# Kernel optimization log

Hardware: AMD Instinct MI355X
Metric: run time of the kernel (lower is better)

## Reference

```python
import jax, jax.numpy as jnp
import numpy as np

B, S, D = 2, 2048, 2048
H = 16
KV_RANK = 512
NOPE, ROPE = 128, 64
QK_HD = NOPE + ROPE  # 192
V_HD = 128
SCALE = QK_HD ** -0.5
EPS = 1.1920929e-07  # torch RMSNorm default eps = finfo(fp32).eps
NEG = -1e9


def rmsnorm(x, w):
    return x * jax.lax.rsqrt(jnp.mean(x * x, axis=-1, keepdims=True) + EPS) * w


def apply_rope(x, freqs):
    # x: (b, s, h, r) interleaved pairs; freqs: (s, r//2) angles
    sh = x.shape
    xr = x.reshape(*sh[:-1], -1, 2)
    a, b = xr[..., 0], xr[..., 1]
    cos = jnp.cos(freqs)[None, :, None, :]
    sin = jnp.sin(freqs)[None, :, None, :]
    return jnp.stack([a * cos - b * sin, a * sin + b * cos], axis=-1).reshape(sh)


def setup_inputs() -> dict:
    key = jax.random.key(0)
    ks = jax.random.split(key, 8)
    inv = lambda k, shape, fan_in: jax.random.uniform(k, shape, jnp.float32, -1.0, 1.0) / np.sqrt(fan_in)
    x = jax.random.normal(ks[0], (B, S, D), jnp.float32)
    freqs = jax.random.uniform(ks[1], (S, ROPE // 2), jnp.float32) * np.float32(np.pi)
    mask = jnp.where(jnp.triu(jnp.ones((S, S), bool), k=1), jnp.float32(NEG), jnp.float32(0.0))
    wq_w = inv(ks[2], (H * QK_HD, D), D)
    wq_b = jnp.zeros((H * QK_HD,), jnp.float32)
    wkv_a_w = inv(ks[3], (KV_RANK + ROPE, D), D)
    wkv_a_b = jnp.zeros((KV_RANK + ROPE,), jnp.float32)
    kv_norm_w = jnp.ones((KV_RANK,), jnp.float32)
    wkv_b_w = inv(ks[4], (H * (NOPE + V_HD), KV_RANK), KV_RANK)
    wo_w = inv(ks[5], (D, H * V_HD), H * V_HD)
    wo_b = jnp.zeros((D,), jnp.float32)
    return dict(x=x, freqs=freqs, mask=mask, wq_w=wq_w, wq_b=wq_b,
                wkv_a_w=wkv_a_w, wkv_a_b=wkv_a_b, kv_norm_w=kv_norm_w,
                wkv_b_w=wkv_b_w, wo_w=wo_w, wo_b=wo_b)


def reference(x, freqs, mask, wq_w, wq_b, wkv_a_w, wkv_a_b, kv_norm_w, wkv_b_w, wo_w, wo_b):
    b, s, _ = x.shape
    # q projection (q_lora_rank == 0 path)
    q = (x @ wq_w.T + wq_b).reshape(b, s, H, QK_HD)
    q_nope, q_pe = q[..., :NOPE], q[..., NOPE:]
    q_pe = apply_rope(q_pe, freqs)
    # latent kv projection
    kv = x @ wkv_a_w.T + wkv_a_b
    kv, k_pe = kv[..., :KV_RANK], kv[..., KV_RANK:]
    k_pe = apply_rope(k_pe[:, :, None, :], freqs)[:, :, 0, :]  # (b, t, r)
    kv_proj = rmsnorm(kv, kv_norm_w)  # (b, t, c)
    wkv_b = wkv_b_w.reshape(H, NOPE + V_HD, KV_RANK)
    # absorb K-nope projection into q
    q_nope = jnp.einsum('bshd,hdc->bshc', q_nope, wkv_b[:, :NOPE])
    scores = (jnp.einsum('bshc,btc->bsht', q_nope, kv_proj)
              + jnp.einsum('bshr,btr->bsht', q_pe, k_pe)) * SCALE
    scores = scores + mask[None, :, None, :]
    scores = jax.nn.softmax(scores.astype(jnp.float32), axis=-1).astype(x.dtype)
    out = jnp.einsum('bsht,btc->bshc', scores, kv_proj)
    out = jnp.einsum('bshc,hdc->bshd', out, wkv_b[:, -V_HD:])
    return out.reshape(b, s, H * V_HD) @ wo_w.T + wo_b
```

## Files before the change

### kernel.cpp

```cpp
#include <hip/hip_runtime.h>
#include <hip/hip_bf16.h>
#include <math.h>

#define B_ 2
#define S_ 2048
#define H_ 16
#define SCALE_ 0.07216878364870323f
#define EPS_ 1.1920929e-07f
#define M0_ 8.0f

typedef __attribute__((ext_vector_type(8))) short bf16x8;
typedef __attribute__((ext_vector_type(4))) float f32x4;
union U4 { uint4 u; bf16x8 v; f32x4 f; };

__device__ __forceinline__ uint bfbits(float x) {
    uint u = __float_as_uint(x);
    return (u + 0x7fffu + ((u >> 16) & 1u)) >> 16;
}
__device__ __forceinline__ uint pack2bf(float a, float b) {
    return bfbits(a) | (bfbits(b) << 16);
}
__device__ __forceinline__ void gld_lds16(const ushort* g, ushort* l) {
    __builtin_amdgcn_global_load_lds(
        (const __attribute__((address_space(1))) uint*)g,
        (__attribute__((address_space(3))) uint*)l, 16, 0, 0);
}

template<bool OUT_BF16>
__global__ __launch_bounds__(256) void mgemm(
    const ushort* __restrict__ A, int lda, long long aOff,
    const ushort* __restrict__ Bm, int ldb, long long bOff,
    const float* __restrict__ bias, float scale,
    void* __restrict__ Cv, int ldc, long long cOff, int K)
{
    __shared__ ushort As[128 * 32];
    __shared__ ushort Bs[128 * 32];

    const int z = blockIdx.z;
    A  += (long long)z * aOff;
    Bm += (long long)z * bOff;

    const int n0 = blockIdx.x * 128;
    const int m0 = blockIdx.y * 128;
    const int tid = threadIdx.x;
    const int w   = tid >> 6;
    const int l   = tid & 63;
    const int m   = l & 15;
    const int q4  = l >> 4;
    const int mw  = (w & 1) * 64;
    const int nw  = (w >> 1) * 64;
    const int sr  = l >> 2;
    const int sc  = l & 3;

    f32x4 acc[4][4];
#pragma unroll
    for (int i = 0; i < 4; ++i)
#pragma unroll
        for (int j = 0; j < 4; ++j) acc[i][j] = (f32x4){0.f, 0.f, 0.f, 0.f};

    for (int k0 = 0; k0 < K; k0 += 32) {
#pragma unroll
        for (int jj = 0; jj < 2; ++jj) {
            const int slot = w * 2 + jj;
            const int row  = slot * 16 + sr;
            const int g    = sc ^ ((row >> 1) & 3);
            gld_lds16(&A[(long long)(m0 + row) * lda + k0 + g * 8], &As[slot * 512]);
            gld_lds16(&Bm[(long long)(n0 + row) * ldb + k0 + g * 8], &Bs[slot * 512]);
        }
        __syncthreads();

        U4 af[4], bf[4];
#pragma unroll
        for (int i = 0; i < 4; ++i) {
            const int ra = mw + i * 16 + m;
            af[i].u = *(const uint4*)&As[ra * 32 + (q4 ^ ((ra >> 1) & 3)) * 8];
            const int rb = nw + i * 16 + m;
            bf[i].u = *(const uint4*)&Bs[rb * 32 + (q4 ^ ((rb >> 1) & 3)) * 8];
        }
#pragma unroll
        for (int i = 0; i < 4; ++i)
#pragma unroll
            for (int j = 0; j < 4; ++j)
                acc[i][j] = __builtin_amdgcn_mfma_f32_16x16x32_bf16(
                    af[i].v, bf[j].v, acc[i][j], 0, 0, 0);
        __syncthreads();
    }

#pragma unroll
    for (int j = 0; j < 4; ++j) {
        const int cn = n0 + nw + j * 16 + m;
        const float bv = bias ? bias[cn] : 0.0f;
#pragma unroll
        for (int i = 0; i < 4; ++i) {
            const int rw = m0 + mw + i * 16 + q4 * 4;
#pragma unroll
            for (int r = 0; r < 4; ++r) {
                const float val = acc[i][j][r] * scale + bv;
                if (OUT_BF16)
                    ((ushort*)Cv)[(long long)z * cOff + (long long)(rw + r) * ldc + cn] =
                        (ushort)bfbits(val);
                else
                    ((float*)Cv)[(long long)z * cOff + (long long)(rw + r) * ldc + cn] = val;
            }
        }
    }
}

__global__ __launch_bounds__(256) void conv_bf16(
    const float* __restrict__ s, ushort* __restrict__ d)
{
    const long long i = ((long long)blockIdx.x * 256 + threadIdx.x) * 4;
    float4 v = *(const float4*)&s[i];
    uint2 p; p.x = pack2bf(v.x, v.y); p.y = pack2bf(v.z, v.w);
    *(uint2*)&d[i] = p;
}

__global__ __launch_bounds__(256) void conv_wkva(
    const float* __restrict__ s, ushort* __restrict__ d)
{
    const int i = (blockIdx.x * 256 + threadIdx.x) * 4;
    const int r = i >> 11;
    uint2 p = make_uint2(0u, 0u);
    if (r < 576) {
        float4 v = *(const float4*)&s[i];
        p.x = pack2bf(v.x, v.y); p.y = pack2bf(v.z, v.w);
    }
    *(uint2*)&d[i] = p;
}

__global__ __launch_bounds__(256) void conv_wkvb_half(
    const float* __restrict__ Wsrc, ushort* __restrict__ V, int rowoff)
{
    const int i = (blockIdx.x * 256 + threadIdx.x) * 4;
    const int h = i >> 16;
    const int rem = i & 65535;
    float4 v = *(const float4*)&Wsrc[((long long)(h * 256 + rowoff)) * 512 + rem];
    uint2 p; p.x = pack2bf(v.x, v.y); p.y = pack2bf(v.z, v.w);
    *(uint2*)&V[i] = p;
}

__global__ __launch_bounds__(256) void conv_qn192(
    const float* __restrict__ q_raw, ushort* __restrict__ q192)
{
    const int i = (blockIdx.x * 256 + threadIdx.x) * 4;
    const int bs = i >> 11;
    const int c = i & 2047;
    const int hh = c >> 7, d = c & 127;
    float4 v = *(const float4*)&q_raw[(long long)bs * 3072 + hh * 192 + d];
    uint2 p;
    p.x = pack2bf(v.x * SCALE_, v.y * SCALE_);
    p.y = pack2bf(v.z * SCALE_, v.w * SCALE_);
    *(uint2*)&q192[((long long)bs * 16 + hh) * 192 + d] = p;
}

__global__ __launch_bounds__(256) void rope_q_kernel(
    const float* __restrict__ q_raw, const float* __restrict__ freqs,
    ushort* __restrict__ q192)
{
    const int idx = blockIdx.x * 256 + threadIdx.x;
    const int i = idx & 31;
    const int h = (idx >> 5) & 15;
    const int s = (idx >> 9) & 2047;
    const int b = idx >> 20;
    const float f = freqs[s * 32 + i];
    float cs, sn;
    __sincosf(f, &sn, &cs);
    const int row = (b * S_ + s) * H_ + h;
    const float a  = q_raw[(long long)(b * S_ + s) * 3072 + h * 192 + 128 + 2 * i];
    const float bb = q_raw[(long long)(b * S_ + s) * 3072 + h * 192 + 128 + 2 * i + 1];
    *(uint*)&q192[(long long)row * 192 + 128 + 2 * i] =
        pack2bf((a * cs - bb * sn) * SCALE_, (a * sn + bb * cs) * SCALE_);
}

__global__ __launch_bounds__(64) void kv_post_kernel(
    const float* __restrict__ kv_raw, const float* __restrict__ bias,
    const float* __restrict__ w, const float* __restrict__ freqs,
    ushort* __restrict__ kv_h)
{
    const int bs = blockIdx.x;
    const int lane = threadIdx.x;
    const float* src = kv_raw + (long long)bs * 640;
    ushort* dst = kv_h + (long long)bs * 576;

    const int c = 4 * lane;
    float4 v0 = *(const float4*)&src[c];
    float4 v1 = *(const float4*)&src[256 + c];
    float4 b0 = *(const float4*)&bias[c];
    float4 b1 = *(const float4*)&bias[256 + c];
    v0.x += b0.x; v0.y += b0.y; v0.z += b0.z; v0.w += b0.w;
    v1.x += b1.x; v1.y += b1.y; v1.z += b1.z; v1.w += b1.w;
    float ss = v0.x * v0.x + v0.y * v0.y + v0.z * v0.z + v0.w * v0.w +
               v1.x * v1.x + v1.y * v1.y + v1.z * v1.z + v1.w * v1.w;
#pragma unroll
    for (int o = 32; o; o >>= 1) ss += __shfl_xor(ss, o, 64);
    const float rs = rsqrtf(ss * (1.0f / 512.0f) + EPS_);

    float4 w0 = *(const float4*)&w[c];
    float4 w1 = *(const float4*)&w[256 + c];
    uint2 p0, p1;
    p0.x = pack2bf(v0.x * rs * w0.x, v0.y * rs * w0.y);
    p0.y = pack2bf(v0.z * rs * w0.z, v0.w * rs * w0.w);
    p1.x = pack2bf(v1.x * rs * w1.x, v1.y * rs * w1.y);
    p1.y = pack2bf(v1.z * rs * w1.z, v1.w * rs * w1.w);
    *(uint2*)&dst[c] = p0;
    *(uint2*)&dst[256 + c] = p1;

    if (lane < 32) {
        const int s = bs & 2047;
        const float f = freqs[s * 32 + lane];
        float cs, sn;
        __sincosf(f, &sn, &cs);
        const float a  = src[512 + 2 * lane]     + bias[512 + 2 * lane];
        const float b2 = src[512 + 2 * lane + 1] + bias[512 + 2 * lane + 1];
        *(uint*)&dst[512 + 2 * lane] = pack2bf(a * cs - b2 * sn, a * sn + b2 * cs);
    }
}

__global__ __launch_bounds__(256) void prep_kimg(
    const ushort* __restrict__ K_h, uint4* __restrict__ khimg)
{
    const int g = blockIdx.x * 256 + threadIdx.x;
    const int lane = g & 63, ck = (g >> 6) & 7, h = (g >> 9) & 15;
    const int tile = (g >> 13) & 63, b = g >> 19;
    const int m = lane & 15, q4 = lane >> 4, f = ck >> 1, s = ck & 1;
    const uint4 v = *(const uint4*)&K_h[
        ((long long)(b * S_ + tile * 32 + s * 16 + m)) * 2048 + h * 128 + f * 32 + q4 * 8];
    khimg[(((long long)(b * 64 + tile) * 16 + h) * 8 + ck) * 64 + lane] = v;
}

__global__ __launch_bounds__(256) void prep_vimg(
    const ushort* __restrict__ V_hT, uint4* __restrict__ vhimg)
{
    const int g = blockIdx.x * 256 + threadIdx.x;
    const int lane = g & 63, c = (g >> 6) & 7, h = (g >> 9) & 15;
    const int tile = (g >> 13) & 63, b = g >> 19;
    const int m = lane & 15, q4 = lane >> 4;
    const uint4 v = *(const uint4*)&V_hT[
        ((long long)((b * 16 + h) * 128 + c * 16 + m)) * 2048 + tile * 32 + q4 * 8];
    vhimg[(((long long)(b * 64 + tile) * 16 + h) * 8 + c) * 64 + lane] = v;
}

__global__ __launch_bounds__(256) void prep_rimg(
    const ushort* __restrict__ kv_h, uint4* __restrict__ rimg)
{
    const int g = blockIdx.x * 256 + threadIdx.x;
    const int lane = g & 63, ck = (g >> 6) & 3, tile = (g >> 8) & 63, b = g >> 14;
    const int m = lane & 15, q4 = lane >> 4, f2 = ck >> 1, s = ck & 1;
    const uint4 v = *(const uint4*)&kv_h[
        ((long long)(b * S_ + tile * 32 + s * 16 + m)) * 576 + 512 + f2 * 32 + q4 * 8];
    rimg[((long long)(b * 64 + tile) * 4 + ck) * 64 + lane] = v;
}

__global__ __launch_bounds__(256, 2) void attn_kernel(
    const ushort* __restrict__ q192,
    const uint4*  __restrict__ khimg,
    const uint4*  __restrict__ rimg,
    const uint4*  __restrict__ vhimg,
    ushort* __restrict__ o_h)
{
    __shared__ uint buf[2][20 * 256];

    const int p    = blockIdx.x;
    const int h    = blockIdx.y;
    const int b    = blockIdx.z;
    const int tid  = threadIdx.x;
    const int wid  = tid >> 6;
    const int lane = tid & 63;
    const int m    = lane & 15;
    const int q4   = lane >> 4;

    auto stage = [&](int bs, int it) {
        const long long tb = (long long)(b * 64 + it);
        const uint4* kb = khimg + ((tb * 16 + h) * 8) * 64;
        const uint4* rb = rimg  + (tb * 4) * 64;
        const uint4* vb = vhimg + ((tb * 16 + h) * 8) * 64;
        ushort* l = (ushort*)&buf[bs][0];
        gld_lds16((const ushort*)(kb + (wid    ) * 64 + lane), l + (wid     ) * 512);
        gld_lds16((const ushort*)(kb + (wid + 4) * 64 + lane), l + (wid +  4) * 512);
        gld_lds16((const ushort*)(rb + (wid    ) * 64 + lane), l + (wid +  8) * 512);
        gld_lds16((const ushort*)(vb + (wid    ) * 64 + lane), l + (wid + 12) * 512);
        gld_lds16((const ushort*)(vb + (wid + 4) * 64 + lane), l + (wid + 16) * 512);
    };

    int cur = 0;
    for (int pass = 0; pass < 2; ++pass) {
        const int chunk = pass ? p : (31 - p);
        const int row0  = chunk * 64 + wid * 16;
        const int sRow  = row0 + m;

        U4 qf[6];
        {
            const uint4* qp = (const uint4*)(q192 + ((long long)(b * S_ + sRow) * H_ + h) * 192);
#pragma unroll
            for (int f = 0; f < 6; ++f) qf[f].u = qp[f * 4 + q4];
        }

        f32x4 o[8];
#pragma unroll
        for (int c = 0; c < 8; ++c) o[c] = (f32x4){0.f, 0.f, 0.f, 0.f};
        float lacc = 0.0f;

        const int nT = chunk * 2 + 2;
        __syncthreads();
        stage(cur, 0);

        for (int it = 0; it < nT; ++it) {
            const int t0 = it * 32;
            __syncthreads();
            if (it + 1 < nT) stage(cur ^ 1, it + 1);
            __builtin_amdgcn_sched_barrier(0);

            if (t0 <= row0 + 15) {
                const uint* bb0 = &buf[cur][0];
                const int abase = lane * 4;

                f32x4 st0 = (f32x4){0.f, 0.f, 0.f, 0.f};
                f32x4 st1 = (f32x4){0.f, 0.f, 0.f, 0.f};
                const bool skip1 = (t0 >= row0);
                if (!skip1) {
#pragma unroll
                    for (int f = 0; f < 6; ++f) {
                        const int ck = (f < 4) ? f * 2 : (f - 4) * 2 + 8;
                        U4 a0, a1;
                        a0.u = *(const uint4*)&bb0[ck * 256 + abase];
                        a1.u = *(const uint4*)&bb0[(ck + 1) * 256 + abase];
                        st0 = __builtin_amdgcn_mfma_f32_16x16x32_bf16(a0.v, qf[f].v, st0, 0, 0, 0);
                        st1 = __builtin_amdgcn_mfma_f32_16x16x32_bf16(a1.v, qf[f].v, st1, 0, 0, 0);
                    }
                } else {
#pragma unroll
                    for (int f = 0; f < 6; ++f) {
                        const int ck = (f < 4) ? f * 2 : (f - 4) * 2 + 8;
                        U4 a0;
                        a0.u = *(const uint4*)&bb0[ck * 256 + abase];
                        st0 = __builtin_amdgcn_mfma_f32_16x16x32_bf16(a0.v, qf[f].v, st0, 0, 0, 0);
                    }
                }

                const int tb0 = t0 + q4 * 4;
                const int tb1 = t0 + 16 + q4 * 4;
                float p00 = (tb0 + 0 <= sRow) ? __expf(st0[0] - M0_) : 0.0f;
                float p01 = (tb0 + 1 <= sRow) ? __expf(st0[1] - M0_) : 0.0f;
                float p02 = (tb0 + 2 <= sRow) ? __expf(st0[2] - M0_) : 0.0f;
                float p03 = (tb0 + 3 <= sRow) ? __expf(st0[3] - M0_) : 0.0f;
                float p10 = (tb1 + 0 <= sRow) ? __expf(st1[0] - M0_) : 0.0f;
                float p11 = (tb1 + 1 <= sRow) ? __expf(st1[1] - M0_) : 0.0f;
                float p12 = (tb1 + 2 <= sRow) ? __expf(st1[2] - M0_) : 0.0f;
                float p13 = (tb1 + 3 <= sRow) ? __expf(st1[3] - M0_) : 0.0f;
                lacc += (p00 + p01) + (p02 + p03) + (p10 + p11) + (p12 + p13);

                U4 bb;
                {
                    uint pk00 = pack2bf(p00, p01);
                    uint pk01 = pack2bf(p02, p03);
                    uint pk10 = pack2bf(p10, p11);
                    uint pk11 = pack2bf(p12, p13);
                    const int srcA = ((lane >> 4) & 1) * 32 + m;
                    const int srcB = srcA + 16;
                    uint a00 = (uint)__shfl((int)pk00, srcA, 64);
                    uint a01 = (uint)__shfl((int)pk01, srcA, 64);
                    uint a10 = (uint)__shfl((int)pk10, srcA, 64);
                    uint a11 = (uint)__shfl((int)pk11, srcA, 64);
                    uint b00 = (uint)__shfl((int)pk00, srcB, 64);
                    uint b01 = (uint)__shfl((int)pk01, srcB, 64);
                    uint b10 = (uint)__shfl((int)pk10, srcB, 64);
                    uint b11 = (uint)__shfl((int)pk11, srcB, 64);
                    const bool hi2 = (lane >> 5) & 1;
                    bb.u.x = hi2 ? a10 : a00;
                    bb.u.y = hi2 ? a11 : a01;
                    bb.u.z = hi2 ? b10 : b00;
                    bb.u.w = hi2 ? b11 : b01;
                }

#pragma unroll
                for (int c = 0; c < 8; ++c) {
                    U4 av; av.u = *(const uint4*)&bb0[(12 + c) * 256 + abase];
                    o[c] = __builtin_amdgcn_mfma_f32_16x16x32_bf16(av.v, bb.v, o[c], 0, 0, 0);
                }
            }
            cur ^= 1;
        }

        lacc += __shfl_xor(lacc, 16, 64);
        lacc += __shfl_xor(lacc, 32, 64);
        const float inv = 1.0f / lacc;

        ushort* op = o_h + ((long long)(b * S_ + sRow) * H_ + h) * 128;
#pragma unroll
        for (int c = 0; c < 8; ++c) {
            uint2 pv;
            pv.x = pack2bf(o[c][0] * inv, o[c][1] * inv);
            pv.y = pack2bf(o[c][2] * inv, o[c][3] * inv);
            *(uint2*)&op[c * 16 + q4 * 4] = pv;
        }
    }
}

extern "C" void kernel_launch(void* const* d_in, const int* in_sizes, int n_in,
                              void* d_out, int out_size, void* d_ws, size_t ws_size,
                              hipStream_t stream)
{
    const float* x         = (const float*)d_in[0];
    const float* freqs     = (const float*)d_in[1];
    const float* wq_w      = (const float*)d_in[3];
    const float* wq_b      = (const float*)d_in[4];
    const float* wkv_a_w   = (const float*)d_in[5];
    const float* wkv_a_b   = (const float*)d_in[6];
    const float* kv_norm_w = (const float*)d_in[7];
    const float* wkv_b_w   = (const float*)d_in[8];
    const float* wo_w      = (const float*)d_in[9];
    const float* wo_b      = (const float*)d_in[10];
    float* out = (float*)d_out;

    char* w = (char*)d_ws;
    ushort* x_bf    = (ushort*)w;  w += 16777216;
    ushort* wq_bf   = (ushort*)w;  w += 12582912;
    ushort* wkva_bf = (ushort*)w;  w += 2621440;
    ushort* wo_bf   = (ushort*)w;  w += 8388608;
    ushort* wkvbK   = (ushort*)w;  w += 2097152;
    ushort* wkvbV   = (ushort*)w;  w += 2097152;
    float*  kv_raw  = (float*)w;   w += 10485760;
    ushort* kv_h    = (ushort*)w;  w += 4718592;
    ushort* K_h     = (ushort*)w;  w += 16777216;
    ushort* V_hT    = (ushort*)w;  w += 16777216;
    uint4*  khimg   = (uint4*)w;   w += 16777216;
    uint4*  vhimg   = (uint4*)w;   w += 16777216;
    uint4*  rimg    = (uint4*)w;   w += 524288;
    char* RA = w;                  w += 50331648;
    float*  q_raw = (float*)RA;
    ushort* o_h   = (ushort*)RA;
    ushort* q192  = (ushort*)w;    w += 25165824;

    dim3 blk(256);

    conv_bf16 <<<dim3(8192), blk, 0, stream>>>(x, x_bf);
    conv_bf16 <<<dim3(6144), blk, 0, stream>>>(wq_w, wq_bf);
    conv_wkva <<<dim3(1280), blk, 0, stream>>>(wkv_a_w, wkva_bf);
    conv_bf16 <<<dim3(4096), blk, 0, stream>>>(wo_w, wo_bf);
    conv_wkvb_half<<<dim3(1024), blk, 0, stream>>>(wkv_b_w, wkvbK, 0);
    conv_wkvb_half<<<dim3(1024), blk, 0, stream>>>(wkv_b_w, wkvbV, 128);

    mgemm<false><<<dim3(24, 32, 1), blk, 0, stream>>>(
        x_bf, 2048, 0LL, wq_bf, 2048, 0LL, wq_b, 1.0f, q_raw, 3072, 0LL, 2048);

    mgemm<false><<<dim3(5, 32, 1), blk, 0, stream>>>(
        x_bf, 2048, 0LL, wkva_bf, 2048, 0LL, nullptr, 1.0f, kv_raw, 640, 0LL, 2048);

    rope_q_kernel<<<dim3(8192), blk, 0, stream>>>(q_raw, freqs, q192);
    conv_qn192<<<dim3(8192), blk, 0, stream>>>(q_raw, q192);

    kv_post_kernel<<<dim3(4096), dim3(64), 0, stream>>>(
        kv_raw, wkv_a_b, kv_norm_w, freqs, kv_h);

    for (int b = 0; b < 2; ++b) {
        mgemm<true><<<dim3(1, 16, 16), blk, 0, stream>>>(
            kv_h + (long long)b * S_ * 576, 576, 0LL,
            wkvbK, 512, 65536LL, nullptr, 1.0f,
            K_h + (long long)b * S_ * 2048, 2048, 128LL, 512);
        mgemm<true><<<dim3(16, 1, 16), blk, 0, stream>>>(
            wkvbV, 512, 65536LL,
            kv_h + (long long)b * S_ * 576, 576, 0LL, nullptr, 1.0f,
            V_hT + (long long)b * 16 * 128 * 2048, 2048, 262144LL, 512);
    }

    prep_kimg<<<dim3(4096), blk, 0, stream>>>(K_h, khimg);
    prep_vimg<<<dim3(4096), blk, 0, stream>>>(V_hT, vhimg);
    prep_rimg<<<dim3(128),  blk, 0, stream>>>(kv_h, rimg);

    attn_kernel<<<dim3(16, 16, 2), blk, 0, stream>>>(q192, khimg, rimg, vhimg, o_h);

    mgemm<false><<<dim3(16, 32, 1), blk, 0, stream>>>(
        o_h, 2048, 0LL, wo_bf, 2048, 0LL, wo_b, 1.0f, out, 2048, 0LL, 2048);
}
```

Baseline: 509.4 us.

## Merge prep kernels, batch GEMMs, and process two row tiles per attention block

Six conversion kernels become one launch, as do the three image-prep kernels and the two q-prep kernels. The per-batch K/V GEMM loop becomes one launch each by giving the GEMM a two-level z offset. The attention kernel now has each wave process two 16-row groups (64 rows apart) over a 128-row chunk, so each staged K/V tile is reused by twice as many rows. It also folds log2(e) into the q scale to use exp2f, uses the hardware bf16 pack instruction, and schedules the largest chunks first. The cost is higher register pressure in attention and a different causal load-balancing scheme.

```diff
diff --git a/kernel.cpp b/kernel.cpp
--- a/kernel.cpp
+++ b/kernel.cpp
@@ -6,6 +6,7 @@
 #define S_ 2048
 #define H_ 16
 #define SCALE_ 0.07216878364870323f
+#define SL2_ (0.07216878364870323f * 1.4426950408889634f)
 #define EPS_ 1.1920929e-07f
 #define M0_ 8.0f
 
@@ -19,6 +20,11 @@
 }
 __device__ __forceinline__ uint pack2bf(float a, float b) {
     return bfbits(a) | (bfbits(b) << 16);
+}
+__device__ __forceinline__ uint cvtpk(float a, float b) {
+    uint r;
+    asm("v_cvt_pk_bf16_f32 %0, %1, %2" : "=v"(r) : "v"(a), "v"(b));
+    return r;
 }
 __device__ __forceinline__ void gld_lds16(const ushort* g, ushort* l) {
     __builtin_amdgcn_global_load_lds(
@@ -28,17 +34,20 @@
 
 template<bool OUT_BF16>
 __global__ __launch_bounds__(256) void mgemm(
-    const ushort* __restrict__ A, int lda, long long aOff,
-    const ushort* __restrict__ Bm, int ldb, long long bOff,
+    const ushort* __restrict__ A, int lda, long long aOff1, long long aOff2,
+    const ushort* __restrict__ Bm, int ldb, long long bOff1, long long bOff2,
     const float* __restrict__ bias, float scale,
-    void* __restrict__ Cv, int ldc, long long cOff, int K)
+    void* __restrict__ Cv, int ldc, long long cOff1, long long cOff2,
+    int K, int zDiv)
 {
     __shared__ ushort As[128 * 32];
     __shared__ ushort Bs[128 * 32];
 
     const int z = blockIdx.z;
-    A  += (long long)z * aOff;
-    Bm += (long long)z * bOff;
+    const int z1 = z % zDiv, z2 = z / zDiv;
+    A  += z1 * aOff1 + z2 * aOff2;
+    Bm += z1 * bOff1 + z2 * bOff2;
+    const long long cBase = z1 * cOff1 + z2 * cOff2;
 
     const int n0 = blockIdx.x * 128;
     const int m0 = blockIdx.y * 128;
@@ -97,79 +106,94 @@
             for (int r = 0; r < 4; ++r) {
                 const float val = acc[i][j][r] * scale + bv;
                 if (OUT_BF16)
-                    ((ushort*)Cv)[(long long)z * cOff + (long long)(rw + r) * ldc + cn] =
+                    ((ushort*)Cv)[cBase + (long long)(rw + r) * ldc + cn] =
                         (ushort)bfbits(val);
                 else
-                    ((float*)Cv)[(long long)z * cOff + (long long)(rw + r) * ldc + cn] = val;
+                    ((float*)Cv)[cBase + (long long)(rw + r) * ldc + cn] = val;
             }
         }
     }
 }
 
-__global__ __launch_bounds__(256) void conv_bf16(
-    const float* __restrict__ s, ushort* __restrict__ d)
-{
-    const long long i = ((long long)blockIdx.x * 256 + threadIdx.x) * 4;
-    float4 v = *(const float4*)&s[i];
-    uint2 p; p.x = pack2bf(v.x, v.y); p.y = pack2bf(v.z, v.w);
-    *(uint2*)&d[i] = p;
-}
-
-__global__ __launch_bounds__(256) void conv_wkva(
-    const float* __restrict__ s, ushort* __restrict__ d)
-{
-    const int i = (blockIdx.x * 256 + threadIdx.x) * 4;
-    const int r = i >> 11;
-    uint2 p = make_uint2(0u, 0u);
-    if (r < 576) {
-        float4 v = *(const float4*)&s[i];
-        p.x = pack2bf(v.x, v.y); p.y = pack2bf(v.z, v.w);
-    }
-    *(uint2*)&d[i] = p;
-}
-
-__global__ __launch_bounds__(256) void conv_wkvb_half(
-    const float* __restrict__ Wsrc, ushort* __restrict__ V, int rowoff)
-{
-    const int i = (blockIdx.x * 256 + threadIdx.x) * 4;
-    const int h = i >> 16;
-    const int rem = i & 65535;
-    float4 v = *(const float4*)&Wsrc[((long long)(h * 256 + rowoff)) * 512 + rem];
-    uint2 p; p.x = pack2bf(v.x, v.y); p.y = pack2bf(v.z, v.w);
-    *(uint2*)&V[i] = p;
-}
-
-__global__ __launch_bounds__(256) void conv_qn192(
-    const float* __restrict__ q_raw, ushort* __restrict__ q192)
-{
-    const int i = (blockIdx.x * 256 + threadIdx.x) * 4;
-    const int bs = i >> 11;
-    const int c = i & 2047;
-    const int hh = c >> 7, d = c & 127;
-    float4 v = *(const float4*)&q_raw[(long long)bs * 3072 + hh * 192 + d];
-    uint2 p;
-    p.x = pack2bf(v.x * SCALE_, v.y * SCALE_);
-    p.y = pack2bf(v.z * SCALE_, v.w * SCALE_);
-    *(uint2*)&q192[((long long)bs * 16 + hh) * 192 + d] = p;
-}
-
-__global__ __launch_bounds__(256) void rope_q_kernel(
+__global__ __launch_bounds__(256) void conv_all(
+    const float* __restrict__ x, const float* __restrict__ wq,
+    const float* __restrict__ wkva, const float* __restrict__ wo,
+    const float* __restrict__ wkvb,
+    ushort* __restrict__ x_bf, ushort* __restrict__ wq_bf,
+    ushort* __restrict__ wkva_bf, ushort* __restrict__ wo_bf,
+    ushort* __restrict__ wkvbK, ushort* __restrict__ wkvbV)
+{
+    const int bid = blockIdx.x;
+    const int tid = threadIdx.x;
+    if (bid < 8192) {
+        const long long i = ((long long)bid * 256 + tid) * 4;
+        float4 v = *(const float4*)&x[i];
+        uint2 p; p.x = pack2bf(v.x, v.y); p.y = pack2bf(v.z, v.w);
+        *(uint2*)&x_bf[i] = p;
+    } else if (bid < 14336) {
+        const long long i = ((long long)(bid - 8192) * 256 + tid) * 4;
+        float4 v = *(const float4*)&wq[i];
+        uint2 p; p.x = pack2bf(v.x, v.y); p.y = pack2bf(v.z, v.w);
+        *(uint2*)&wq_bf[i] = p;
+    } else if (bid < 15616) {
+        const int i = ((bid - 14336) * 256 + tid) * 4;
+        const int r = i >> 11;
+        uint2 p = make_uint2(0u, 0u);
+        if (r < 576) {
+            float4 v = *(const float4*)&wkva[i];
+            p.x = pack2bf(v.x, v.y); p.y = pack2bf(v.z, v.w);
+        }
+        *(uint2*)&wkva_bf[i] = p;
+    } else if (bid < 19712) {
+        const long long i = ((long long)(bid - 15616) * 256 + tid) * 4;
+        float4 v = *(const float4*)&wo[i];
+        uint2 p; p.x = pack2bf(v.x, v.y); p.y = pack2bf(v.z, v.w);
+        *(uint2*)&wo_bf[i] = p;
+    } else if (bid < 20736) {
+        const int i = ((bid - 19712) * 256 + tid) * 4;
+        const int h = i >> 16, rem = i & 65535;
+        float4 v = *(const float4*)&wkvb[((long long)(h * 256)) * 512 + rem];
+        uint2 p; p.x = pack2bf(v.x, v.y); p.y = pack2bf(v.z, v.w);
+        *(uint2*)&wkvbK[i] = p;
+    } else {
+        const int i = ((bid - 20736) * 256 + tid) * 4;
+        const int h = i >> 16, rem = i & 65535;
+        float4 v = *(const float4*)&wkvb[((long long)(h * 256 + 128)) * 512 + rem];
+        uint2 p; p.x = pack2bf(v.x, v.y); p.y = pack2bf(v.z, v.w);
+        *(uint2*)&wkvbV[i] = p;
+    }
+}
+
+__global__ __launch_bounds__(256) void qprep(
     const float* __restrict__ q_raw, const float* __restrict__ freqs,
     ushort* __restrict__ q192)
 {
     const int idx = blockIdx.x * 256 + threadIdx.x;
-    const int i = idx & 31;
-    const int h = (idx >> 5) & 15;
-    const int s = (idx >> 9) & 2047;
-    const int b = idx >> 20;
-    const float f = freqs[s * 32 + i];
-    float cs, sn;
-    __sincosf(f, &sn, &cs);
-    const int row = (b * S_ + s) * H_ + h;
-    const float a  = q_raw[(long long)(b * S_ + s) * 3072 + h * 192 + 128 + 2 * i];
-    const float bb = q_raw[(long long)(b * S_ + s) * 3072 + h * 192 + 128 + 2 * i + 1];
-    *(uint*)&q192[(long long)row * 192 + 128 + 2 * i] =
-        pack2bf((a * cs - bb * sn) * SCALE_, (a * sn + bb * cs) * SCALE_);
+    const int row = idx / 48;
+    const int c4  = idx % 48;
+    const int bs = row >> 4, h = row & 15;
+    const float* src = q_raw + (long long)bs * 3072 + h * 192;
+    if (c4 < 32) {
+        const int d = c4 * 4;
+        float4 v = *(const float4*)&src[d];
+        uint2 p;
+        p.x = pack2bf(v.x * SL2_, v.y * SL2_);
+        p.y = pack2bf(v.z * SL2_, v.w * SL2_);
+        *(uint2*)&q192[(long long)row * 192 + d] = p;
+    } else {
+        const int j = c4 - 32;
+        const int s = bs & 2047;
+        const float f0 = freqs[s * 32 + j * 2];
+        const float f1 = freqs[s * 32 + j * 2 + 1];
+        float c0, s0, c1, s1;
+        __sincosf(f0, &s0, &c0);
+        __sincosf(f1, &s1, &c1);
+        float4 v = *(const float4*)&src[128 + j * 4];
+        uint2 p;
+        p.x = pack2bf((v.x * c0 - v.y * s0) * SL2_, (v.x * s0 + v.y * c0) * SL2_);
+        p.y = pack2bf((v.z * c1 - v.w * s1) * SL2_, (v.z * s1 + v.w * c1) * SL2_);
+        *(uint2*)&q192[(long long)row * 192 + 128 + j * 4] = p;
+    }
 }
 
 __global__ __launch_bounds__(64) void kv_post_kernel(
@@ -216,39 +240,37 @@
     }
 }
 
-__global__ __launch_bounds__(256) void prep_kimg(
-    const ushort* __restrict__ K_h, uint4* __restrict__ khimg)
-{
-    const int g = blockIdx.x * 256 + threadIdx.x;
-    const int lane = g & 63, ck = (g >> 6) & 7, h = (g >> 9) & 15;
-    const int tile = (g >> 13) & 63, b = g >> 19;
-    const int m = lane & 15, q4 = lane >> 4, f = ck >> 1, s = ck & 1;
-    const uint4 v = *(const uint4*)&K_h[
-        ((long long)(b * S_ + tile * 32 + s * 16 + m)) * 2048 + h * 128 + f * 32 + q4 * 8];
-    khimg[(((long long)(b * 64 + tile) * 16 + h) * 8 + ck) * 64 + lane] = v;
-}
-
-__global__ __launch_bounds__(256) void prep_vimg(
-    const ushort* __restrict__ V_hT, uint4* __restrict__ vhimg)
-{
-    const int g = blockIdx.x * 256 + threadIdx.x;
-    const int lane = g & 63, c = (g >> 6) & 7, h = (g >> 9) & 15;
-    const int tile = (g >> 13) & 63, b = g >> 19;
-    const int m = lane & 15, q4 = lane >> 4;
-    const uint4 v = *(const uint4*)&V_hT[
-        ((long long)((b * 16 + h) * 128 + c * 16 + m)) * 2048 + tile * 32 + q4 * 8];
-    vhimg[(((long long)(b * 64 + tile) * 16 + h) * 8 + c) * 64 + lane] = v;
-}
-
-__global__ __launch_bounds__(256) void prep_rimg(
-    const ushort* __restrict__ kv_h, uint4* __restrict__ rimg)
-{
-    const int g = blockIdx.x * 256 + threadIdx.x;
-    const int lane = g & 63, ck = (g >> 6) & 3, tile = (g >> 8) & 63, b = g >> 14;
-    const int m = lane & 15, q4 = lane >> 4, f2 = ck >> 1, s = ck & 1;
-    const uint4 v = *(const uint4*)&kv_h[
-        ((long long)(b * S_ + tile * 32 + s * 16 + m)) * 576 + 512 + f2 * 32 + q4 * 8];
-    rimg[((long long)(b * 64 + tile) * 4 + ck) * 64 + lane] = v;
+__global__ __launch_bounds__(256) void prep_all(
+    const ushort* __restrict__ K_h, const ushort* __restrict__ V_hT,
+    const ushort* __restrict__ kv_h,
+    uint4* __restrict__ khimg, uint4* __restrict__ vhimg,
+    uint4* __restrict__ rimg)
+{
+    const int bid = blockIdx.x;
+    if (bid < 4096) {
+        const int g = bid * 256 + threadIdx.x;
+        const int lane = g & 63, ck = (g >> 6) & 7, h = (g >> 9) & 15;
+        const int tile = (g >> 13) & 63, b = g >> 19;
+        const int m = lane & 15, q4 = lane >> 4, f = ck >> 1, s = ck & 1;
+        const uint4 v = *(const uint4*)&K_h[
+            ((long long)(b * S_ + tile * 32 + s * 16 + m)) * 2048 + h * 128 + f * 32 + q4 * 8];
+        khimg[(((long long)(b * 64 + tile) * 16 + h) * 8 + ck) * 64 + lane] = v;
+    } else if (bid < 8192) {
+        const int g = (bid - 4096) * 256 + threadIdx.x;
+        const int lane = g & 63, c = (g >> 6) & 7, h = (g >> 9) & 15;
+        const int tile = (g >> 13) & 63, b = g >> 19;
+        const int m = lane & 15, q4 = lane >> 4;
+        const uint4 v = *(const uint4*)&V_hT[
+            ((long long)((b * 16 + h) * 128 + c * 16 + m)) * 2048 + tile * 32 + q4 * 8];
+        vhimg[(((long long)(b * 64 + tile) * 16 + h) * 8 + c) * 64 + lane] = v;
+    } else {
+        const int g = (bid - 8192) * 256 + threadIdx.x;
+        const int lane = g & 63, ck = (g >> 6) & 3, tile = (g >> 8) & 63, b = g >> 14;
+        const int m = lane & 15, q4 = lane >> 4, f2 = ck >> 1, s = ck & 1;
+        const uint4 v = *(const uint4*)&kv_h[
+            ((long long)(b * S_ + tile * 32 + s * 16 + m)) * 576 + 512 + f2 * 32 + q4 * 8];
+        rimg[((long long)(b * 64 + tile) * 4 + ck) * 64 + lane] = v;
+    }
 }
 
 __global__ __launch_bounds__(256, 2) void attn_kernel(
@@ -260,14 +282,20 @@
 {
     __shared__ uint buf[2][20 * 256];
 
-    const int p    = blockIdx.x;
-    const int h    = blockIdx.y;
-    const int b    = blockIdx.z;
+    const int hb   = blockIdx.x;
+    const int h    = hb & 15;
+    const int b    = hb >> 4;
+    const int chunk = 15 - (int)blockIdx.y;
     const int tid  = threadIdx.x;
     const int wid  = tid >> 6;
     const int lane = tid & 63;
     const int m    = lane & 15;
     const int q4   = lane >> 4;
+
+    const int row0a = chunk * 128 + wid * 16;
+    const int row0b = row0a + 64;
+    const int sRa   = row0a + m;
+    const int sRb   = row0b + m;
 
     auto stage = [&](int bs, int it) {
         const long long tb = (long long)(b * 64 + it);
@@ -282,117 +310,157 @@
         gld_lds16((const ushort*)(vb + (wid + 4) * 64 + lane), l + (wid + 16) * 512);
     };
 
+    U4 qfa[6], qfb[6];
+    {
+        const uint4* qpa = (const uint4*)(q192 + ((long long)(b * S_ + sRa) * H_ + h) * 192);
+        const uint4* qpb = (const uint4*)(q192 + ((long long)(b * S_ + sRb) * H_ + h) * 192);
+#pragma unroll
+        for (int f = 0; f < 6; ++f) { qfa[f].u = qpa[f * 4 + q4]; qfb[f].u = qpb[f * 4 + q4]; }
+    }
+
+    f32x4 oA[8], oB[8];
+#pragma unroll
+    for (int c = 0; c < 8; ++c) {
+        oA[c] = (f32x4){0.f, 0.f, 0.f, 0.f};
+        oB[c] = (f32x4){0.f, 0.f, 0.f, 0.f};
+    }
+    float lA = 0.0f, lB = 0.0f;
+
+    auto softpack = [&](const f32x4 s0, const f32x4 s1, int t0v, int rw0,
+                        float& lac) -> U4 {
+        float p00, p01, p02, p03, p10, p11, p12, p13;
+        if (t0v + 31 <= rw0) {
+            p00 = exp2f(s0[0] - M0_); p01 = exp2f(s0[1] - M0_);
+            p02 = exp2f(s0[2] - M0_); p03 = exp2f(s0[3] - M0_);
+            p10 = exp2f(s1[0] - M0_); p11 = exp2f(s1[1] - M0_);
+            p12 = exp2f(s1[2] - M0_); p13 = exp2f(s1[3] - M0_);
+        } else {
+            const int sR = rw0 + m;
+            const int tb0 = t0v + q4 * 4;
+            const int tb1 = tb0 + 16;
+            p00 = (tb0 + 0 <= sR) ? exp2f(s0[0] - M0_) : 0.0f;
+            p01 = (tb0 + 1 <= sR) ? exp2f(s0[1] - M0_) : 0.0f;
+            p02 = (tb0 + 2 <= sR) ? exp2f(s0[2] - M0_) : 0.0f;
+            p03 = (tb0 + 3 <= sR) ? exp2f(s0[3] - M0_) : 0.0f;
+            p10 = (tb1 + 0 <= sR) ? exp2f(s1[0] - M0_) : 0.0f;
+            p11 = (tb1 + 1 <= sR) ? exp2f(s1[1] - M0_) : 0.0f;
+            p12 = (tb1 + 2 <= sR) ? exp2f(s1[2] - M0_) : 0.0f;
+            p13 = (tb1 + 3 <= sR) ? exp2f(s1[3] - M0_) : 0.0f;
+        }
+        lac += (p00 + p01) + (p02 + p03) + (p10 + p11) + (p12 + p13);
+        U4 bb;
+        {
+            uint pk00 = cvtpk(p00, p01);
+            uint pk01 = cvtpk(p02, p03);
+            uint pk10 = cvtpk(p10, p11);
+            uint pk11 = cvtpk(p12, p13);
+            const int srcA = ((lane >> 4) & 1) * 32 + m;
+            const int srcB = srcA + 16;
+            uint a00 = (uint)__shfl((int)pk00, srcA, 64);
+            uint a01 = (uint)__shfl((int)pk01, srcA, 64);
+            uint a10 = (uint)__shfl((int)pk10, srcA, 64);
+            uint a11 = (uint)__shfl((int)pk11, srcA, 64);
+            uint b00 = (uint)__shfl((int)pk00, srcB, 64);
+            uint b01 = (uint)__shfl((int)pk01, srcB, 64);
+            uint b10 = (uint)__shfl((int)pk10, srcB, 64);
+            uint b11 = (uint)__shfl((int)pk11, srcB, 64);
+            const bool hi2 = (lane >> 5) & 1;
+            bb.u.x = hi2 ? a10 : a00;
+            bb.u.y = hi2 ? a11 : a01;
+            bb.u.z = hi2 ? b10 : b00;
+            bb.u.w = hi2 ? b11 : b01;
+        }
+        return bb;
+    };
+
+    const int nT = chunk * 4 + 4;
+    stage(0, 0);
     int cur = 0;
-    for (int pass = 0; pass < 2; ++pass) {
-        const int chunk = pass ? p : (31 - p);
-        const int row0  = chunk * 64 + wid * 16;
-        const int sRow  = row0 + m;
-
-        U4 qf[6];
-        {
-            const uint4* qp = (const uint4*)(q192 + ((long long)(b * S_ + sRow) * H_ + h) * 192);
-#pragma unroll
-            for (int f = 0; f < 6; ++f) qf[f].u = qp[f * 4 + q4];
-        }
-
-        f32x4 o[8];
-#pragma unroll
-        for (int c = 0; c < 8; ++c) o[c] = (f32x4){0.f, 0.f, 0.f, 0.f};
-        float lacc = 0.0f;
-
-        const int nT = chunk * 2 + 2;
+
+    for (int it = 0; it < nT; ++it) {
+        const int t0 = it * 32;
         __syncthreads();
-        stage(cur, 0);
-
-        for (int it = 0; it < nT; ++it) {
-            const int t0 = it * 32;
-            __syncthreads();
-            if (it + 1 < nT) stage(cur ^ 1, it + 1);
-            __builtin_amdgcn_sched_barrier(0);
-
-            if (t0 <= row0 + 15) {
-                const uint* bb0 = &buf[cur][0];
-                const int abase = lane * 4;
-
-                f32x4 st0 = (f32x4){0.f, 0.f, 0.f, 0.f};
-                f32x4 st1 = (f32x4){0.f, 0.f, 0.f, 0.f};
-                const bool skip1 = (t0 >= row0);
-                if (!skip1) {
-#pragma unroll
-                    for (int f = 0; f < 6; ++f) {
-                        const int ck = (f < 4) ? f * 2 : (f - 4) * 2 + 8;
-                        U4 a0, a1;
-                        a0.u = *(const uint4*)&bb0[ck * 256 + abase];
+        if (it + 1 < nT) stage(cur ^ 1, it + 1);
+        __builtin_amdgcn_sched_barrier(0);
+
+        const uint* bb0 = &buf[cur][0];
+        const int abase = lane * 4;
+        const bool liveB = (t0 <= row0b + 15);
+        const bool liveA = (t0 <= row0a + 15);
+        const bool twoA  = (t0 < row0a);
+        const bool twoB  = (t0 < row0b);
+
+        if (liveB) {
+            f32x4 sA0 = (f32x4){0.f,0.f,0.f,0.f}, sA1 = (f32x4){0.f,0.f,0.f,0.f};
+            f32x4 sB0 = (f32x4){0.f,0.f,0.f,0.f}, sB1 = (f32x4){0.f,0.f,0.f,0.f};
+
+            if (twoA) {
+#pragma unroll
+                for (int f = 0; f < 6; ++f) {
+                    const int ck = (f < 4) ? f * 2 : (f - 4) * 2 + 8;
+                    U4 a0, a1;
+                    a0.u = *(const uint4*)&bb0[ck * 256 + abase];
+                    a1.u = *(const uint4*)&bb0[(ck + 1) * 256 + abase];
+                    sA0 = __builtin_amdgcn_mfma_f32_16x16x32_bf16(a0.v, qfa[f].v, sA0, 0, 0, 0);
+                    sB0 = __builtin_amdgcn_mfma_f32_16x16x32_bf16(a0.v, qfb[f].v, sB0, 0, 0, 0);
+                    sA1 = __builtin_amdgcn_mfma_f32_16x16x32_bf16(a1.v, qfa[f].v, sA1, 0, 0, 0);
+                    sB1 = __builtin_amdgcn_mfma_f32_16x16x32_bf16(a1.v, qfb[f].v, sB1, 0, 0, 0);
+                }
+            } else {
+#pragma unroll
+                for (int f = 0; f < 6; ++f) {
+                    const int ck = (f < 4) ? f * 2 : (f - 4) * 2 + 8;
+                    U4 a0;
+                    a0.u = *(const uint4*)&bb0[ck * 256 + abase];
+                    if (liveA)
+                        sA0 = __builtin_amdgcn_mfma_f32_16x16x32_bf16(a0.v, qfa[f].v, sA0, 0, 0, 0);
+                    sB0 = __builtin_amdgcn_mfma_f32_16x16x32_bf16(a0.v, qfb[f].v, sB0, 0, 0, 0);
+                    if (twoB) {
+                        U4 a1;
                         a1.u = *(const uint4*)&bb0[(ck + 1) * 256 + abase];
-                        st0 = __builtin_amdgcn_mfma_f32_16x16x32_bf16(a0.v, qf[f].v, st0, 0, 0, 0);
-                        st1 = __builtin_amdgcn_mfma_f32_16x16x32_bf16(a1.v, qf[f].v, st1, 0, 0, 0);
-                    }
-                } else {
-#pragma unroll
-                    for (int f = 0; f < 6; ++f) {
-                        const int ck = (f < 4) ? f * 2 : (f - 4) * 2 + 8;
-                        U4 a0;
-                        a0.u = *(const uint4*)&bb0[ck * 256 + abase];
-                        st0 = __builtin_amdgcn_mfma_f32_16x16x32_bf16(a0.v, qf[f].v, st0, 0, 0, 0);
+                        sB1 = __builtin_amdgcn_mfma_f32_16x16x32_bf16(a1.v, qfb[f].v, sB1, 0, 0, 0);
                     }
                 }
-
-                const int tb0 = t0 + q4 * 4;
-                const int tb1 = t0 + 16 + q4 * 4;
-                float p00 = (tb0 + 0 <= sRow) ? __expf(st0[0] - M0_) : 0.0f;
-                float p01 = (tb0 + 1 <= sRow) ? __expf(st0[1] - M0_) : 0.0f;
-                float p02 = (tb0 + 2 <= sRow) ? __expf(st0[2] - M0_) : 0.0f;
-                float p03 = (tb0 + 3 <= sRow) ? __expf(st0[3] - M0_) : 0.0f;
-                float p10 = (tb1 + 0 <= sRow) ? __expf(st1[0] - M0_) : 0.0f;
-                float p11 = (tb1 + 1 <= sRow) ? __expf(st1[1] - M0_) : 0.0f;
-                float p12 = (tb1 + 2 <= sRow) ? __expf(st1[2] - M0_) : 0.0f;
-                float p13 = (tb1 + 3 <= sRow) ? __expf(st1[3] - M0_) : 0.0f;
-                lacc += (p00 + p01) + (p02 + p03) + (p10 + p11) + (p12 + p13);
-
-                U4 bb;
-                {
-                    uint pk00 = pack2bf(p00, p01);
-                    uint pk01 = pack2bf(p02, p03);
-                    uint pk10 = pack2bf(p10, p11);
-                    uint pk11 = pack2bf(p12, p13);
-                    const int srcA = ((lane >> 4) & 1) * 32 + m;
-                    const int srcB = srcA + 16;
-                    uint a00 = (uint)__shfl((int)pk00, srcA, 64);
-                    uint a01 = (uint)__shfl((int)pk01, srcA, 64);
-                    uint a10 = (uint)__shfl((int)pk10, srcA, 64);
-                    uint a11 = (uint)__shfl((int)pk11, srcA, 64);
-                    uint b00 = (uint)__shfl((int)pk00, srcB, 64);
-                    uint b01 = (uint)__shfl((int)pk01, srcB, 64);
-                    uint b10 = (uint)__shfl((int)pk10, srcB, 64);
-                    uint b11 = (uint)__shfl((int)pk11, srcB, 64);
-                    const bool hi2 = (lane >> 5) & 1;
-                    bb.u.x = hi2 ? a10 : a00;
-                    bb.u.y = hi2 ? a11 : a01;
-                    bb.u.z = hi2 ? b10 : b00;
-                    bb.u.w = hi2 ? b11 : b01;
-                }
-
+            }
+
+            U4 bbB = softpack(sB0, sB1, t0, row0b, lB);
+            if (liveA) {
+                U4 bbA = softpack(sA0, sA1, t0, row0a, lA);
 #pragma unroll
                 for (int c = 0; c < 8; ++c) {
                     U4 av; av.u = *(const uint4*)&bb0[(12 + c) * 256 + abase];
-                    o[c] = __builtin_amdgcn_mfma_f32_16x16x32_bf16(av.v, bb.v, o[c], 0, 0, 0);
+                    oB[c] = __builtin_amdgcn_mfma_f32_16x16x32_bf16(av.v, bbB.v, oB[c], 0, 0, 0);
+                    oA[c] = __builtin_amdgcn_mfma_f32_16x16x32_bf16(av.v, bbA.v, oA[c], 0, 0, 0);
+                }
+            } else {
+#pragma unroll
+                for (int c = 0; c < 8; ++c) {
+                    U4 av; av.u = *(const uint4*)&bb0[(12 + c) * 256 + abase];
+                    oB[c] = __builtin_amdgcn_mfma_f32_16x16x32_bf16(av.v, bbB.v, oB[c], 0, 0, 0);
                 }
             }
-            cur ^= 1;
-        }
-
-        lacc += __shfl_xor(lacc, 16, 64);
-        lacc += __shfl_xor(lacc, 32, 64);
-        const float inv = 1.0f / lacc;
-
-        ushort* op = o_h + ((long long)(b * S_ + sRow) * H_ + h) * 128;
-#pragma unroll
-        for (int c = 0; c < 8; ++c) {
-            uint2 pv;
-            pv.x = pack2bf(o[c][0] * inv, o[c][1] * inv);
-            pv.y = pack2bf(o[c][2] * inv, o[c][3] * inv);
-            *(uint2*)&op[c * 16 + q4 * 4] = pv;
-        }
+        }
+        cur ^= 1;
+    }
+
+    lA += __shfl_xor(lA, 16, 64);
+    lA += __shfl_xor(lA, 32, 64);
+    lB += __shfl_xor(lB, 16, 64);
+    lB += __shfl_xor(lB, 32, 64);
+    const float invA = 1.0f / lA;
+    const float invB = 1.0f / lB;
+
+    ushort* opa = o_h + ((long long)(b * S_ + sRa) * H_ + h) * 128;
+    ushort* opb = o_h + ((long long)(b * S_ + sRb) * H_ + h) * 128;
+#pragma unroll
+    for (int c = 0; c < 8; ++c) {
+        uint2 pva, pvb;
+        pva.x = cvtpk(oA[c][0] * invA, oA[c][1] * invA);
+        pva.y = cvtpk(oA[c][2] * invA, oA[c][3] * invA);
+        pvb.x = cvtpk(oB[c][0] * invB, oB[c][1] * invB);
+        pvb.y = cvtpk(oB[c][2] * invB, oB[c][3] * invB);
+        *(uint2*)&opa[c * 16 + q4 * 4] = pva;
+        *(uint2*)&opb[c * 16 + q4 * 4] = pvb;
     }
 }
 
@@ -433,42 +501,37 @@
 
     dim3 blk(256);
 
-    conv_bf16 <<<dim3(8192), blk, 0, stream>>>(x, x_bf);
-    conv_bf16 <<<dim3(6144), blk, 0, stream>>>(wq_w, wq_bf);
-    conv_wkva <<<dim3(1280), blk, 0, stream>>>(wkv_a_w, wkva_bf);
-    conv_bf16 <<<dim3(4096), blk, 0, stream>>>(wo_w, wo_bf);
-    conv_wkvb_half<<<dim3(1024), blk, 0, stream>>>(wkv_b_w, wkvbK, 0);
-    conv_wkvb_half<<<dim3(1024), blk, 0, stream>>>(wkv_b_w, wkvbV, 128);
+    conv_all<<<dim3(21760), blk, 0, stream>>>(
+        x, wq_w, wkv_a_w, wo_w, wkv_b_w,
+        x_bf, wq_bf, wkva_bf, wo_bf, wkvbK, wkvbV);
 
     mgemm<false><<<dim3(24, 32, 1), blk, 0, stream>>>(
-        x_bf, 2048, 0LL, wq_bf, 2048, 0LL, wq_b, 1.0f, q_raw, 3072, 0LL, 2048);
+        x_bf, 2048, 0LL, 0LL, wq_bf, 2048, 0LL, 0LL, wq_b, 1.0f,
+        q_raw, 3072, 0LL, 0LL, 2048, 1);
 
     mgemm<false><<<dim3(5, 32, 1), blk, 0, stream>>>(
-        x_bf, 2048, 0LL, wkva_bf, 2048, 0LL, nullptr, 1.0f, kv_raw, 640, 0LL, 2048);
-
-    rope_q_kernel<<<dim3(8192), blk, 0, stream>>>(q_raw, freqs, q192);
-    conv_qn192<<<dim3(8192), blk, 0, stream>>>(q_raw, q192);
+        x_bf, 2048, 0LL, 0LL, wkva_bf, 2048, 0LL, 0LL, nullptr, 1.0f,
+        kv_raw, 640, 0LL, 0LL, 2048, 1);
+
+    qprep<<<dim3(12288), blk, 0, stream>>>(q_raw, freqs, q192);
 
     kv_post_kernel<<<dim3(4096), dim3(64), 0, stream>>>(
         kv_raw, wkv_a_b, kv_norm_w, freqs, kv_h);
 
-    for (int b = 0; b < 2; ++b) {
-        mgemm<true><<<dim3(1, 16, 16), blk, 0, stream>>>(
-            kv_h + (long long)b * S_ * 576, 576, 0LL,
-            wkvbK, 512, 65536LL, nullptr, 1.0f,
-            K_h + (long long)b * S_ * 2048, 2048, 128LL, 512);
-        mgemm<true><<<dim3(16, 1, 16), blk, 0, stream>>>(
-            wkvbV, 512, 65536LL,
-            kv_h + (long long)b * S_ * 576, 576, 0LL, nullptr, 1.0f,
-            V_hT + (long long)b * 16 * 128 * 2048, 2048, 262144LL, 512);
-    }
-
-    prep_kimg<<<dim3(4096), blk, 0, stream>>>(K_h, khimg);
-    prep_vimg<<<dim3(4096), blk, 0, stream>>>(V_hT, vhimg);
-    prep_rimg<<<dim3(128),  blk, 0, stream>>>(kv_h, rimg);
-
-    attn_kernel<<<dim3(16, 16, 2), blk, 0, stream>>>(q192, khimg, rimg, vhimg, o_h);
+    mgemm<true><<<dim3(1, 16, 32), blk, 0, stream>>>(
+        kv_h, 576, 0LL, (long long)S_ * 576,
+        wkvbK, 512, 65536LL, 0LL, nullptr, 1.0f,
+        K_h, 2048, 128LL, (long long)S_ * 2048, 512, 16);
+    mgemm<true><<<dim3(16, 1, 32), blk, 0, stream>>>(
+        wkvbV, 512, 65536LL, 0LL,
+        kv_h, 576, 0LL, (long long)S_ * 576, nullptr, 1.0f,
+        V_hT, 2048, 262144LL, 4194304LL, 512, 16);
+
+    prep_all<<<dim3(8320), blk, 0, stream>>>(K_h, V_hT, kv_h, khimg, vhimg, rimg);
+
+    attn_kernel<<<dim3(32, 16, 1), blk, 0, stream>>>(q192, khimg, rimg, vhimg, o_h);
 
     mgemm<false><<<dim3(16, 32, 1), blk, 0, stream>>>(
-        o_h, 2048, 0LL, wo_bf, 2048, 0LL, wo_b, 1.0f, out, 2048, 0LL, 2048);
-}
+        o_h, 2048, 0LL, 0LL, wo_bf, 2048, 0LL, 0LL, wo_b, 1.0f,
+        out, 2048, 0LL, 0LL, 2048, 1);
+}
```

After: 491.1 us. -3.6%, faster.
